# Kernel tuning notes

Measured on AMD Instinct MI355X. Metric: run time of the kernel, lower is better.

Reference implementation:

```python
import jax, jax.numpy as jnp
import numpy as np

IN_DIMS = 32
HID = 64
N_HIDDEN = 5  # tcnn n_hidden_layers = hidden_layers + 1 = 5
OUT_DIMS = 3
BATCH = 2097152


def setup_inputs() -> dict:
    key = jax.random.key(0)
    ks = jax.random.split(key, N_HIDDEN + 2)
    x = jax.random.normal(ks[0], (BATCH, IN_DIMS), dtype=jnp.float32)
    # tcnn FullyFusedMLP has no biases; Kaiming-ish init scale
    W0 = jax.random.normal(ks[1], (IN_DIMS, HID), dtype=jnp.float32) * (1.0 / np.sqrt(IN_DIMS))
    Wh = jax.random.normal(ks[2], (N_HIDDEN - 1, HID, HID), dtype=jnp.float32) * (1.0 / np.sqrt(HID))
    Wo = jax.random.normal(ks[3], (HID, OUT_DIMS), dtype=jnp.float32) * (1.0 / np.sqrt(HID))
    return {"x": x, "W0": W0, "Wh": Wh, "Wo": Wo}


def reference(x, W0, Wh, Wo):
    # input layer -> ReLU
    h = jax.nn.relu(x @ W0)  # [B, 64]
    # 4 more hidden layers of 64->64 with ReLU (small fixed count, unrolled)
    for i in range(Wh.shape[0]):
        h = jax.nn.relu(h @ Wh[i])
    # linear output layer (output_activation = None)
    return h @ Wo  # [B, 3]
```

## Files before the change

### kernel.cpp

```cpp
#include <hip/hip_runtime.h>


typedef __attribute__((ext_vector_type(8))) short short8;
typedef __attribute__((ext_vector_type(4))) float f32x4;

#define BATCH   2097152
#define NBLOCKS 1024
#define WAVES   (NBLOCKS * 4)
#define ROWS_PW 32
#define ITERS   (BATCH / (WAVES * ROWS_PW))
#define RSTRIDE 144
#define BUFSZ   (16 * RSTRIDE)
static_assert(BATCH == (size_t)WAVES * ROWS_PW * ITERS, "");

__device__ __forceinline__ unsigned cvt_pk(float a, float b) {
    unsigned r;
    asm("v_cvt_pk_bf16_f32 %0, %1, %2" : "=v"(r) : "v"(a), "v"(b));
    return r;
}

__global__ __launch_bounds__(256, 2)
void mlp_fused(const float* __restrict__ x, const float* __restrict__ W0,
               const float* __restrict__ Wh, const float* __restrict__ Wo,
               float* __restrict__ out)
{
    __shared__ __align__(16) unsigned char smem[4 * 2 * BUFSZ];

    const int tid  = threadIdx.x;
    const int w    = tid >> 6;
    const int lane = tid & 63;
    const int n = lane & 15;
    const int q = lane >> 4;

    short8 wf0[4], wfh[4][4][2], wfo[2];
    #pragma unroll
    for (int t = 0; t < 4; ++t) {
        const float* p = W0 + (8 * q) * 64 + 16 * t + n;
        union { unsigned u[4]; short8 s; } f;
        #pragma unroll
        for (int i = 0; i < 4; ++i)
            f.u[i] = cvt_pk(p[(2 * i) * 64], p[(2 * i + 1) * 64]);
        wf0[t] = f.s;
    }
    #pragma unroll
    for (int l = 0; l < 4; ++l)
        #pragma unroll
        for (int t = 0; t < 4; ++t)
            #pragma unroll
            for (int c = 0; c < 2; ++c) {
                const float* p = Wh + l * 4096 + (32 * c + 8 * q) * 64 + 16 * t + n;
                union { unsigned u[4]; short8 s; } f;
                #pragma unroll
                for (int i = 0; i < 4; ++i)
                    f.u[i] = cvt_pk(p[(2 * i) * 64], p[(2 * i + 1) * 64]);
                wfh[l][t][c] = f.s;
            }
    #pragma unroll
    for (int c = 0; c < 2; ++c) {
        union { unsigned u[4]; short8 s; } f;
        #pragma unroll
        for (int i = 0; i < 4; ++i) {
            float a = (n < 3) ? Wo[(32 * c + 8 * q + 2 * i)     * 3 + n] : 0.f;
            float b = (n < 3) ? Wo[(32 * c + 8 * q + 2 * i + 1) * 3 + n] : 0.f;
            f.u[i] = cvt_pk(a, b);
        }
        wfo[c] = f.s;
    }

    unsigned char* const bufA = smem + w * (2 * BUFSZ);
    unsigned char* const bufB = bufA + BUFSZ;
    const unsigned aw = (unsigned)n * RSTRIDE + 8u  * (unsigned)q;
    const unsigned ar = (unsigned)n * RSTRIDE + 16u * (unsigned)q;

    const int gw = blockIdx.x * 4 + w;
    const f32x4 z = {0.f, 0.f, 0.f, 0.f};

    f32x4 rawA[2], rawB[2];
    auto issue_x = [&](int it) {
        const size_t r = ((size_t)it * WAVES + gw) * ROWS_PW;
        const f32x4* pA = (const f32x4*)(x + (r + n) * 32) + 2 * q;
        rawA[0] = pA[0]; rawA[1] = pA[1];
        const f32x4* pB = (const f32x4*)(x + (r + 16 + n) * 32) + 2 * q;
        rawB[0] = pB[0]; rawB[1] = pB[1];
    };
    auto convert_x = [&](const f32x4* raw) -> short8 {
        union { unsigned u[4]; short8 s; } f;
        f.u[0] = cvt_pk(raw[0][0], raw[0][1]);
        f.u[1] = cvt_pk(raw[0][2], raw[0][3]);
        f.u[2] = cvt_pk(raw[1][0], raw[1][1]);
        f.u[3] = cvt_pk(raw[1][2], raw[1][3]);
        return f.s;
    };
    auto stage = [&](const f32x4 (&acc)[4], unsigned char* buf,
                     short8& b0, short8& b1) {
        #pragma unroll
        for (int t = 0; t < 4; ++t) {
            uint2 wv;
            wv.x = cvt_pk(fmaxf(acc[t][0], 0.f), fmaxf(acc[t][1], 0.f));
            wv.y = cvt_pk(fmaxf(acc[t][2], 0.f), fmaxf(acc[t][3], 0.f));
            *(uint2*)(buf + aw + 32u * t) = wv;
        }
        b0 = *(const short8*)(buf + ar);
        b1 = *(const short8*)(buf + ar + 64u);
    };

    issue_x(0);

    #pragma unroll 1
    for (int it = 0; it < ITERS; ++it) {
        const short8 xfA = convert_x(rawA);
        const short8 xfB = convert_x(rawB);
        if (it + 1 < ITERS) issue_x(it + 1);

        const size_t row0 = ((size_t)it * WAVES + gw) * ROWS_PW;

        f32x4 accA[4], accB[4];
        #pragma unroll
        for (int t = 0; t < 4; ++t)
            accA[t] = __builtin_amdgcn_mfma_f32_16x16x32_bf16(wf0[t], xfA, z, 0, 0, 0);
        #pragma unroll
        for (int t = 0; t < 4; ++t)
            accB[t] = __builtin_amdgcn_mfma_f32_16x16x32_bf16(wf0[t], xfB, z, 0, 0, 0);

        #pragma unroll
        for (int s = 0; s < 4; ++s) {
            short8 a0, a1, c0, c1;
            stage(accA, bufA, a0, a1);
            stage(accB, bufB, c0, c1);
            #pragma unroll
            for (int t = 0; t < 4; ++t)
                accA[t] = __builtin_amdgcn_mfma_f32_16x16x32_bf16(
                              wfh[s][t][0], a0, z, 0, 0, 0);
            #pragma unroll
            for (int t = 0; t < 4; ++t)
                accA[t] = __builtin_amdgcn_mfma_f32_16x16x32_bf16(
                              wfh[s][t][1], a1, accA[t], 0, 0, 0);
            #pragma unroll
            for (int t = 0; t < 4; ++t)
                accB[t] = __builtin_amdgcn_mfma_f32_16x16x32_bf16(
                              wfh[s][t][0], c0, z, 0, 0, 0);
            #pragma unroll
            for (int t = 0; t < 4; ++t)
                accB[t] = __builtin_amdgcn_mfma_f32_16x16x32_bf16(
                              wfh[s][t][1], c1, accB[t], 0, 0, 0);
        }

        {
            short8 a0, a1, c0, c1;
            stage(accA, bufA, a0, a1);
            stage(accB, bufB, c0, c1);
            f32x4 oA = __builtin_amdgcn_mfma_f32_16x16x32_bf16(wfo[0], a0, z, 0, 0, 0);
            oA = __builtin_amdgcn_mfma_f32_16x16x32_bf16(wfo[1], a1, oA, 0, 0, 0);
            f32x4 oB = __builtin_amdgcn_mfma_f32_16x16x32_bf16(wfo[0], c0, z, 0, 0, 0);
            oB = __builtin_amdgcn_mfma_f32_16x16x32_bf16(wfo[1], c1, oB, 0, 0, 0);
            if (lane < 16) {
                float* pA = out + (row0 + lane) * 3;
                pA[0] = oA[0]; pA[1] = oA[1]; pA[2] = oA[2];
                float* pB = out + (row0 + 16 + lane) * 3;
                pB[0] = oB[0]; pB[1] = oB[1]; pB[2] = oB[2];
            }
        }
    }
}

extern "C" void kernel_launch(void* const* d_in, const int* in_sizes, int n_in,
                              void* d_out, int out_size, void* d_ws, size_t ws_size,
                              hipStream_t stream) {
    (void)in_sizes; (void)n_in; (void)d_ws; (void)ws_size; (void)out_size;
    const float* x  = (const float*)d_in[0];
    const float* W0 = (const float*)d_in[1];
    const float* Wh = (const float*)d_in[2];
    const float* Wo = (const float*)d_in[3];
    float* out = (float*)d_out;
    mlp_fused<<<NBLOCKS, 256, 0, stream>>>(x, W0, Wh, Wo, out);
}
```

Baseline: 386.0 us.

## Permute weight columns so MFMA outputs feed next layer directly in registers

Reorders the output-neuron columns of the hidden and input weight fragments with a permutation phi, so each lane's MFMA accumulator values already sit in the K-layout the next layer's B operand expects. This removes the LDS write/read round trip between layers, and the shared-memory buffer with it, packing activations with cvt_pk straight into registers. The cost is a less obvious index mapping that must match the MFMA layouts exactly, or results will be wrong.

New measurement: 383.2 us. Within noise of the previous version (-0.7%).

```diff
diff --git a/kernel.cpp b/kernel.cpp
--- a/kernel.cpp
+++ b/kernel.cpp
@@ -9,8 +9,6 @@
 #define WAVES   (NBLOCKS * 4)
 #define ROWS_PW 32
 #define ITERS   (BATCH / (WAVES * ROWS_PW))
-#define RSTRIDE 144
-#define BUFSZ   (16 * RSTRIDE)
 static_assert(BATCH == (size_t)WAVES * ROWS_PW * ITERS, "");
 
 __device__ __forceinline__ unsigned cvt_pk(float a, float b) {
@@ -24,18 +22,21 @@
                const float* __restrict__ Wh, const float* __restrict__ Wo,
                float* __restrict__ out)
 {
-    __shared__ __align__(16) unsigned char smem[4 * 2 * BUFSZ];
-
     const int tid  = threadIdx.x;
     const int w    = tid >> 6;
     const int lane = tid & 63;
     const int n = lane & 15;
     const int q = lane >> 4;
 
+    int phi[4];
+    #pragma unroll
+    for (int t = 0; t < 4; ++t)
+        phi[t] = 32 * (t >> 1) + 8 * (n >> 2) + 4 * (t & 1) + (n & 3);
+
     short8 wf0[4], wfh[4][4][2], wfo[2];
     #pragma unroll
     for (int t = 0; t < 4; ++t) {
-        const float* p = W0 + (8 * q) * 64 + 16 * t + n;
+        const float* p = W0 + (8 * q) * 64 + phi[t];
         union { unsigned u[4]; short8 s; } f;
         #pragma unroll
         for (int i = 0; i < 4; ++i)
@@ -48,7 +49,7 @@
         for (int t = 0; t < 4; ++t)
             #pragma unroll
             for (int c = 0; c < 2; ++c) {
-                const float* p = Wh + l * 4096 + (32 * c + 8 * q) * 64 + 16 * t + n;
+                const float* p = Wh + l * 4096 + (32 * c + 8 * q) * 64 + phi[t];
                 union { unsigned u[4]; short8 s; } f;
                 #pragma unroll
                 for (int i = 0; i < 4; ++i)
@@ -66,11 +67,6 @@
         }
         wfo[c] = f.s;
     }
-
-    unsigned char* const bufA = smem + w * (2 * BUFSZ);
-    unsigned char* const bufB = bufA + BUFSZ;
-    const unsigned aw = (unsigned)n * RSTRIDE + 8u  * (unsigned)q;
-    const unsigned ar = (unsigned)n * RSTRIDE + 16u * (unsigned)q;
 
     const int gw = blockIdx.x * 4 + w;
     const f32x4 z = {0.f, 0.f, 0.f, 0.f};
@@ -91,17 +87,17 @@
         f.u[3] = cvt_pk(raw[1][2], raw[1][3]);
         return f.s;
     };
-    auto stage = [&](const f32x4 (&acc)[4], unsigned char* buf,
-                     short8& b0, short8& b1) {
-        #pragma unroll
-        for (int t = 0; t < 4; ++t) {
-            uint2 wv;
-            wv.x = cvt_pk(fmaxf(acc[t][0], 0.f), fmaxf(acc[t][1], 0.f));
-            wv.y = cvt_pk(fmaxf(acc[t][2], 0.f), fmaxf(acc[t][3], 0.f));
-            *(uint2*)(buf + aw + 32u * t) = wv;
-        }
-        b0 = *(const short8*)(buf + ar);
-        b1 = *(const short8*)(buf + ar + 64u);
+    auto packact = [&](const f32x4 (&acc)[4], short8& b0, short8& b1) {
+        union { unsigned u[4]; short8 s; } A, B;
+        A.u[0] = cvt_pk(fmaxf(acc[0][0], 0.f), fmaxf(acc[0][1], 0.f));
+        A.u[1] = cvt_pk(fmaxf(acc[0][2], 0.f), fmaxf(acc[0][3], 0.f));
+        A.u[2] = cvt_pk(fmaxf(acc[1][0], 0.f), fmaxf(acc[1][1], 0.f));
+        A.u[3] = cvt_pk(fmaxf(acc[1][2], 0.f), fmaxf(acc[1][3], 0.f));
+        B.u[0] = cvt_pk(fmaxf(acc[2][0], 0.f), fmaxf(acc[2][1], 0.f));
+        B.u[1] = cvt_pk(fmaxf(acc[2][2], 0.f), fmaxf(acc[2][3], 0.f));
+        B.u[2] = cvt_pk(fmaxf(acc[3][0], 0.f), fmaxf(acc[3][1], 0.f));
+        B.u[3] = cvt_pk(fmaxf(acc[3][2], 0.f), fmaxf(acc[3][3], 0.f));
+        b0 = A.s; b1 = B.s;
     };
 
     issue_x(0);
@@ -125,8 +121,8 @@
         #pragma unroll
         for (int s = 0; s < 4; ++s) {
             short8 a0, a1, c0, c1;
-            stage(accA, bufA, a0, a1);
-            stage(accB, bufB, c0, c1);
+            packact(accA, a0, a1);
+            packact(accB, c0, c1);
             #pragma unroll
             for (int t = 0; t < 4; ++t)
                 accA[t] = __builtin_amdgcn_mfma_f32_16x16x32_bf16(
@@ -147,8 +143,8 @@
 
         {
             short8 a0, a1, c0, c1;
-            stage(accA, bufA, a0, a1);
-            stage(accB, bufB, c0, c1);
+            packact(accA, a0, a1);
+            packact(accB, c0, c1);
             f32x4 oA = __builtin_amdgcn_mfma_f32_16x16x32_bf16(wfo[0], a0, z, 0, 0, 0);
             oA = __builtin_amdgcn_mfma_f32_16x16x32_bf16(wfo[1], a1, oA, 0, 0, 0);
             f32x4 oB = __builtin_amdgcn_mfma_f32_16x16x32_bf16(wfo[0], c0, z, 0, 0, 0);
```
